# Kernel tuning notes

Measured on AMD Instinct MI355X. Metric: run time of the kernel, lower is better.

The kernel has to match this reference:

```python
import jax, jax.numpy as jnp
import numpy as np

LEAKY_SLOPE = 0.01  # torch nn.LeakyReLU default


def leaky_relu(x):
    return jnp.where(x >= 0, x, LEAKY_SLOPE * x)


def rgcn_conv(x, edge_index, edge_type, w_rel, w_root, b_conv):
    # PyG RGCNConv: out = x @ W_root + b + sum_r mean_{edges of rel r into i}(x_src @ W_r)
    n = x.shape[0]
    src, dst = edge_index[0], edge_index[1]
    out = x @ w_root + b_conv
    num_rel = w_rel.shape[0]
    for r in range(num_rel):  # small fixed relation count
        mask = (edge_type == r)
        msg = x[src] @ w_rel[r]                      # [E, H]
        msg = jnp.where(mask[:, None], msg, 0.0)
        agg = jax.ops.segment_sum(msg, dst, num_segments=n)          # [N, H]
        cnt = jax.ops.segment_sum(mask.astype(x.dtype), dst, num_segments=n)
        out = out + agg / jnp.maximum(cnt, 1.0)[:, None]             # mean aggr
    return out


def setup_inputs() -> dict:
    key = jax.random.key(0)
    ks = jax.random.split(key, 10)
    N, E, D_IN, H, OUT, R = 50000, 600000, 768, 128, 3, 2
    s_in = 1.0 / np.sqrt(D_IN)
    s_h = 1.0 / np.sqrt(H)
    return {
        "feature": jax.random.normal(ks[0], (N, D_IN), dtype=jnp.float32),
        "edge_index": jax.random.randint(ks[1], (2, E), 0, N, dtype=jnp.int64),
        "edge_type": jax.random.randint(ks[2], (E,), 0, R, dtype=jnp.int64),
        "w_in": jax.random.uniform(ks[3], (D_IN, H), jnp.float32, -s_in, s_in),
        "b_in": jax.random.uniform(ks[4], (H,), jnp.float32, -s_in, s_in),
        "w_rel": jax.random.uniform(ks[5], (R, H, H), jnp.float32, -s_h, s_h),
        "w_root": jax.random.uniform(ks[6], (H, H), jnp.float32, -s_h, s_h),
        "b_conv": jnp.zeros((H,), jnp.float32),
        "w_out": jax.random.uniform(ks[7], (H, OUT), jnp.float32, -s_h, s_h),
        "b_out": jax.random.uniform(ks[8], (OUT,), jnp.float32, -s_h, s_h),
    }


def reference(feature, edge_index, edge_type, w_in, b_in, w_rel, w_root, b_conv, w_out, b_out):
    x = leaky_relu(feature @ w_in + b_in)
    # NOTE: original forward applies rgcn1 twice (shared weights); dropout is
    # identity at inference; rgcn2/linear_relu_output1 are unused.
    x = rgcn_conv(x, edge_index, edge_type, w_rel, w_root, b_conv)
    x = rgcn_conv(x, edge_index, edge_type, w_rel, w_root, b_conv)
    return x @ w_out + b_out
```

## Files before the change

### kernel.cpp

```cpp
#include <hip/hip_runtime.h>

#define H 128
#define CAP 64

typedef _Float16 f16x8 __attribute__((ext_vector_type(8)));
typedef float    f32x4 __attribute__((ext_vector_type(4)));

__global__ __launch_bounds__(256) void hist_fill(const int* __restrict__ src,
    const int* __restrict__ dst, const int* __restrict__ et,
    int* __restrict__ cnt, int* __restrict__ elist, int E, int N)
{
    int e = blockIdx.x * 256 + threadIdx.x;
    if (e >= E) return;
    int s = src[e], d = dst[e], t = et[e];
    int b = t * N + d;
    int pos = atomicAdd(&cnt[b], 1);
    if (pos < CAP) elist[(size_t)b * CAP + pos] = s;
}

__global__ __launch_bounds__(256) void prep_w(const float* __restrict__ w_in,
    const float* __restrict__ w_root, const float* __restrict__ w_rel,
    _Float16* __restrict__ wInT, _Float16* __restrict__ w3T, int K)
{
    int idx = blockIdx.x * 256 + threadIdx.x;
    int tot1 = K * H;
    if (idx < tot1) {
        int c = idx / K, k = idx - c * K;
        wInT[idx] = (_Float16)w_in[(size_t)k * H + c];
    } else {
        int i2 = idx - tot1;
        if (i2 < 3 * H * H) {
            int m = i2 / (H * H), r2 = i2 - m * (H * H);
            int c = r2 >> 7, k = r2 & 127;
            const float* s = (m == 0) ? w_root : (w_rel + (size_t)(m - 1) * H * H);
            w3T[i2] = (_Float16)s[(size_t)k * H + c];
        }
    }
}

__device__ __forceinline__ f16x8 cvt8(float4 v0, float4 v1) {
    f16x8 t;
    t[0] = (_Float16)v0.x; t[1] = (_Float16)v0.y; t[2] = (_Float16)v0.z; t[3] = (_Float16)v0.w;
    t[4] = (_Float16)v1.x; t[5] = (_Float16)v1.y; t[6] = (_Float16)v1.z; t[7] = (_Float16)v1.w;
    return t;
}

__global__ __launch_bounds__(256, 4) void gemm_big(const float* __restrict__ A,
    const _Float16* __restrict__ WT, const float* __restrict__ bias,
    _Float16* __restrict__ C16, int M, int K)
{
    __shared__ _Float16 As[2][64][40];
    __shared__ _Float16 Bs[2][128][40];

    const int tid = threadIdx.x;
    const int bm  = blockIdx.x * 64;
    const int w   = tid >> 6;
    const int l   = tid & 63;
    const int l15 = l & 15;
    const int q   = l >> 4;
    const int wr  = (w & 1) * 32;
    const int wc  = (w >> 1) * 64;

    const int sar = tid >> 2;
    const int sak = (tid & 3) * 8;
    int sarow = bm + sar; if (sarow >= M) sarow = M - 1;
    const float* ap = A + (size_t)sarow * K + sak;
    const int sbc = tid >> 1;
    const int sbk = (tid & 1) * 16;
    const _Float16* wp = WT + (size_t)sbc * K + sbk;

    f32x4 acc[2][4];
    const f32x4 z4 = {0.f, 0.f, 0.f, 0.f};
#pragma unroll
    for (int i = 0; i < 2; i++)
#pragma unroll
        for (int j = 0; j < 4; j++) acc[i][j] = z4;

    {
        float4 a0 = *(const float4*)(ap);
        float4 a1 = *(const float4*)(ap + 4);
        f16x8 b0  = *(const f16x8*)(wp);
        f16x8 b1  = *(const f16x8*)(wp + 8);
        *(f16x8*)&As[0][sar][sak]     = cvt8(a0, a1);
        *(f16x8*)&Bs[0][sbc][sbk]     = b0;
        *(f16x8*)&Bs[0][sbc][sbk + 8] = b1;
    }
    __syncthreads();

    const int steps = K / 32;
#pragma unroll 2
    for (int s = 0; s < steps; s++) {
        const int cur = s & 1;
        const bool more = (s + 1) < steps;
        float4 na0, na1; f16x8 nb0, nb1;
        if (more) {
            const int k0 = (s + 1) * 32;
            na0 = *(const float4*)(ap + k0);
            na1 = *(const float4*)(ap + k0 + 4);
            nb0 = *(const f16x8*)(wp + k0);
            nb1 = *(const f16x8*)(wp + k0 + 8);
        }
        f16x8 af[2], bf[4];
#pragma unroll
        for (int i = 0; i < 2; i++) af[i] = *(const f16x8*)&As[cur][wr + i * 16 + l15][q * 8];
#pragma unroll
        for (int j = 0; j < 4; j++) bf[j] = *(const f16x8*)&Bs[cur][wc + j * 16 + l15][q * 8];
#pragma unroll
        for (int i = 0; i < 2; i++)
#pragma unroll
            for (int j = 0; j < 4; j++)
                acc[i][j] = __builtin_amdgcn_mfma_f32_16x16x32_f16(af[i], bf[j], acc[i][j], 0, 0, 0);
        if (more) {
            *(f16x8*)&As[cur ^ 1][sar][sak]     = cvt8(na0, na1);
            *(f16x8*)&Bs[cur ^ 1][sbc][sbk]     = nb0;
            *(f16x8*)&Bs[cur ^ 1][sbc][sbk + 8] = nb1;
        }
        __syncthreads();
    }

#pragma unroll
    for (int j = 0; j < 4; j++) {
        int col = wc + j * 16 + l15;
        float bj = bias[col];
#pragma unroll
        for (int i = 0; i < 2; i++)
#pragma unroll
            for (int rg = 0; rg < 4; rg++) {
                int row = bm + wr + i * 16 + q * 4 + rg;
                if (row < M) {
                    float v = acc[i][j][rg] + bj;
                    v = (v >= 0.f) ? v : 0.01f * v;
                    C16[(size_t)row * H + col] = (_Float16)v;
                }
            }
    }
}

__global__ __launch_bounds__(512) void gemm3(const _Float16* __restrict__ X16,
    const _Float16* __restrict__ W3, const float* __restrict__ bias,
    float* __restrict__ Y, _Float16* __restrict__ Hh, int M, int mtiles,
    size_t NH)
{
    const int w   = threadIdx.x >> 6;
    const int l   = threadIdx.x & 63;
    const int l15 = l & 15;
    const int q   = l >> 4;
    const int col = w * 16 + l15;

    f16x8 bf[3][4];
#pragma unroll
    for (int m = 0; m < 3; m++) {
        const _Float16* wpp = W3 + (size_t)m * H * H + (size_t)col * H + q * 8;
#pragma unroll
        for (int c = 0; c < 4; c++) bf[m][c] = *(const f16x8*)(wpp + c * 32);
    }
    const float bj = bias[col];

    int t = blockIdx.x;
    if (t >= mtiles) return;
    f16x8 xf[4];
    {
        const _Float16* xp = X16 + ((size_t)t * 16 + l15) * H + q * 8;
#pragma unroll
        for (int c = 0; c < 4; c++) xf[c] = *(const f16x8*)(xp + c * 32);
    }

    const f32x4 z4 = {0.f, 0.f, 0.f, 0.f};
    while (true) {
        int tn = t + gridDim.x;
        bool more = tn < mtiles;
        f16x8 xnf[4];
        if (more) {
            const _Float16* xp = X16 + ((size_t)tn * 16 + l15) * H + q * 8;
#pragma unroll
            for (int c = 0; c < 4; c++) xnf[c] = *(const f16x8*)(xp + c * 32);
        }

        f32x4 a0 = z4, a1 = z4, a2 = z4;
#pragma unroll
        for (int c = 0; c < 4; c++) {
            a0 = __builtin_amdgcn_mfma_f32_16x16x32_f16(xf[c], bf[0][c], a0, 0, 0, 0);
            a1 = __builtin_amdgcn_mfma_f32_16x16x32_f16(xf[c], bf[1][c], a1, 0, 0, 0);
            a2 = __builtin_amdgcn_mfma_f32_16x16x32_f16(xf[c], bf[2][c], a2, 0, 0, 0);
        }

#pragma unroll
        for (int rg = 0; rg < 4; rg++) {
            int row = t * 16 + q * 4 + rg;
            if (row < M) {
                Y [(size_t)row * H + col]      = a0[rg] + bj;
                Hh[(size_t)row * H + col]      = (_Float16)a1[rg];
                Hh[NH + (size_t)row * H + col] = (_Float16)a2[rg];
            }
        }
        if (!more) break;
        t = tn;
#pragma unroll
        for (int c = 0; c < 4; c++) xf[c] = xnf[c];
    }
}

__global__ __launch_bounds__(256) void gather_mean(const float* __restrict__ Y,
    const _Float16* __restrict__ h, const int* __restrict__ elist,
    const int* __restrict__ cnt, _Float16* __restrict__ xn, int N, size_t NH)
{
    int wv = blockIdx.x * 4 + (threadIdx.x >> 6);
    int l  = threadIdx.x & 63;
    if (wv >= N) return;

    int d0r = cnt[wv], d1r = cnt[N + wv];
    int d0 = d0r < CAP ? d0r : CAP;
    int d1 = d1r < CAP ? d1r : CAP;
    float inv0 = d0r > 0 ? 1.f / (float)d0r : 0.f;
    float inv1 = d1r > 0 ? 1.f / (float)d1r : 0.f;
    const int* l0 = elist + (size_t)wv * CAP;
    const int* l1 = elist + ((size_t)N + wv) * CAP;
    const int tot = d0 + d1;

    const int eo = l >> 4;
    const int c8 = (l & 15) * 8;

    float acc[8];
#pragma unroll
    for (int j = 0; j < 8; j++) acc[j] = 0.f;

    for (int p = eo; p < tot; p += 8) {
        int pb = p + 4;
        bool fA = p < d0;
        int   sA  = fA ? l0[p] : l1[p - d0];
        float scA = fA ? inv0 : inv1;
        size_t hA = fA ? (size_t)0 : NH;
        f16x8 vA  = *(const f16x8*)&h[hA + (size_t)sA * H + c8];
        if (pb < tot) {
            bool fB = pb < d0;
            int   sB  = fB ? l0[pb] : l1[pb - d0];
            float scB = fB ? inv0 : inv1;
            size_t hB = fB ? (size_t)0 : NH;
            f16x8 vB  = *(const f16x8*)&h[hB + (size_t)sB * H + c8];
#pragma unroll
            for (int j = 0; j < 8; j++) acc[j] += scA * (float)vA[j] + scB * (float)vB[j];
        } else {
#pragma unroll
            for (int j = 0; j < 8; j++) acc[j] += scA * (float)vA[j];
        }
    }

#pragma unroll
    for (int j = 0; j < 8; j++) {
        acc[j] += __shfl_xor(acc[j], 16);
        acc[j] += __shfl_xor(acc[j], 32);
    }

    if (eo == 0) {
        float4 y0 = *(const float4*)&Y[(size_t)wv * H + c8];
        float4 y1 = *(const float4*)&Y[(size_t)wv * H + c8 + 4];
        f16x8 o;
        o[0] = (_Float16)(acc[0] + y0.x); o[1] = (_Float16)(acc[1] + y0.y);
        o[2] = (_Float16)(acc[2] + y0.z); o[3] = (_Float16)(acc[3] + y0.w);
        o[4] = (_Float16)(acc[4] + y1.x); o[5] = (_Float16)(acc[5] + y1.y);
        o[6] = (_Float16)(acc[6] + y1.z); o[7] = (_Float16)(acc[7] + y1.w);
        *(f16x8*)&xn[(size_t)wv * H + c8] = o;
    }
}

__global__ __launch_bounds__(256) void out_gemm(const _Float16* __restrict__ X16,
    const float* __restrict__ Wo, const float* __restrict__ bo,
    float* __restrict__ out, int N, int OUT)
{
    int row = blockIdx.x * 4 + (threadIdx.x >> 6);
    int lane = threadIdx.x & 63;
    if (row >= N) return;
    float a0 = (float)X16[(size_t)row * H + lane];
    float a1 = (float)X16[(size_t)row * H + 64 + lane];
    for (int c = 0; c < OUT; c++) {
        float p = a0 * Wo[lane * OUT + c] + a1 * Wo[(64 + lane) * OUT + c];
        for (int off = 32; off > 0; off >>= 1) p += __shfl_down(p, off);
        if (lane == 0) out[(size_t)row * OUT + c] = p + bo[c];
    }
}

extern "C" void kernel_launch(void* const* d_in, const int* in_sizes, int n_in,
                              void* d_out, int out_size, void* d_ws, size_t ws_size,
                              hipStream_t stream) {
    const float* feature = (const float*)d_in[0];
    const int*   ei      = (const int*)d_in[1];
    const int*   et      = (const int*)d_in[2];
    const float* w_in    = (const float*)d_in[3];
    const float* b_in    = (const float*)d_in[4];
    const float* w_rel   = (const float*)d_in[5];
    const float* w_root  = (const float*)d_in[6];
    const float* b_conv  = (const float*)d_in[7];
    const float* w_out   = (const float*)d_in[8];
    const float* b_out   = (const float*)d_in[9];

    const int HH   = in_sizes[4];
    const int D_IN = in_sizes[3] / HH;
    const int N    = in_sizes[0] / D_IN;
    const int E    = in_sizes[1] / 2;
    const int R    = in_sizes[5] / (HH * HH);
    const int OUT  = in_sizes[9];

    const size_t NH = (size_t)N * H;

    char* base = (char*)d_ws;
    _Float16* wInT = (_Float16*)base;
    _Float16* w3T  = wInT + (size_t)D_IN * HH;
    _Float16* x0   = w3T + (size_t)3 * HH * HH;
    _Float16* x1   = x0 + NH;
    _Float16* h    = x1 + NH;
    float* y       = (float*)(h + (size_t)R * NH);
    int* cnt       = (int*)(y + NH);
    int* elist     = cnt + (size_t)R * N;

    hipMemsetAsync(cnt, 0, sizeof(int) * (size_t)R * N, stream);
    prep_w<<<(D_IN * HH + 3 * HH * HH + 255) / 256, 256, 0, stream>>>(
        w_in, w_root, w_rel, wInT, w3T, D_IN);
    hist_fill<<<(E + 255) / 256, 256, 0, stream>>>(ei, ei + E, et, cnt, elist, E, N);

    gemm_big<<<(N + 63) / 64, 256, 0, stream>>>(feature, wInT, b_in, x0, N, D_IN);

    const int mtiles = (N + 15) / 16;
    _Float16* xc = x0;
    _Float16* xo = x1;
    for (int layer = 0; layer < 2; layer++) {
        gemm3<<<1024, 512, 0, stream>>>(xc, w3T, b_conv, y, h, N, mtiles, NH);
        gather_mean<<<(N + 3) / 4, 256, 0, stream>>>(y, h, elist, cnt, xo, N, NH);
        _Float16* t = xc; xc = xo; xo = t;
    }

    out_gemm<<<(N + 3) / 4, 256, 0, stream>>>(xc, w_out, b_out, (float*)d_out, N, OUT);
}
```

Before: 464.8 us.

## Split-K input GEMM with LDS-resident weight half and separate reduce kernel

Reworks the first dense GEMM so each 1024-thread block holds one K-half of the transposed weight in shared memory. Each wave streams its A rows straight from global memory into registers, so the A tile is no longer staged through LDS and no per-step barriers are needed. Each block writes fp32 partial sums for its K-half, and a new reduce kernel adds the two halves, applies bias and LeakyReLU, and converts to fp16. This removes the LDS double-buffer for A and the repeated weight reloads, at the cost of writing and reading two fp32 N×H partial buffers plus one extra launch.

```diff
diff --git a/kernel.cpp b/kernel.cpp
--- a/kernel.cpp
+++ b/kernel.cpp
@@ -2,6 +2,7 @@
 
 #define H 128
 #define CAP 64
+#define BSTRIDE 392
 
 typedef _Float16 f16x8 __attribute__((ext_vector_type(8)));
 typedef float    f32x4 __attribute__((ext_vector_type(4)));
@@ -45,95 +46,98 @@
     return t;
 }
 
-__global__ __launch_bounds__(256, 4) void gemm_big(const float* __restrict__ A,
-    const _Float16* __restrict__ WT, const float* __restrict__ bias,
-    _Float16* __restrict__ C16, int M, int K)
-{
-    __shared__ _Float16 As[2][64][40];
-    __shared__ _Float16 Bs[2][128][40];
-
-    const int tid = threadIdx.x;
-    const int bm  = blockIdx.x * 64;
+__global__ __launch_bounds__(1024, 4) void gemm_big(const float* __restrict__ A,
+    const _Float16* __restrict__ WT, float* __restrict__ P,
+    int M, int K, size_t NH)
+{
+    __shared__ _Float16 Bsh[128 * BSTRIDE];
+
+    const int khalf = blockIdx.x & 1;
+    const int rt    = blockIdx.x >> 1;
+    const int KH    = K >> 1;
+    const int tid   = threadIdx.x;
+
+    {
+        const int col = tid >> 3;
+        const int seg = tid & 7;
+        const _Float16* srcp = WT + (size_t)col * K + khalf * KH + seg * 8;
+        _Float16* dstp = &Bsh[col * BSTRIDE + seg * 8];
+        for (int k = 0; k < KH; k += 64)
+            *(f16x8*)(dstp + k) = *(const f16x8*)(srcp + k);
+    }
+    __syncthreads();
+
     const int w   = tid >> 6;
     const int l   = tid & 63;
     const int l15 = l & 15;
     const int q   = l >> 4;
-    const int wr  = (w & 1) * 32;
-    const int wc  = (w >> 1) * 64;
-
-    const int sar = tid >> 2;
-    const int sak = (tid & 3) * 8;
-    int sarow = bm + sar; if (sarow >= M) sarow = M - 1;
-    const float* ap = A + (size_t)sarow * K + sak;
-    const int sbc = tid >> 1;
-    const int sbk = (tid & 1) * 16;
-    const _Float16* wp = WT + (size_t)sbc * K + sbk;
-
-    f32x4 acc[2][4];
+
+    int arow = rt * 256 + w * 16 + l15;
+    if (arow >= M) arow = M - 1;
+    const float* ap = A + (size_t)arow * K + khalf * KH + q * 8;
+
+    f32x4 acc[8];
     const f32x4 z4 = {0.f, 0.f, 0.f, 0.f};
 #pragma unroll
-    for (int i = 0; i < 2; i++)
-#pragma unroll
-        for (int j = 0; j < 4; j++) acc[i][j] = z4;
-
-    {
-        float4 a0 = *(const float4*)(ap);
-        float4 a1 = *(const float4*)(ap + 4);
-        f16x8 b0  = *(const f16x8*)(wp);
-        f16x8 b1  = *(const f16x8*)(wp + 8);
-        *(f16x8*)&As[0][sar][sak]     = cvt8(a0, a1);
-        *(f16x8*)&Bs[0][sbc][sbk]     = b0;
-        *(f16x8*)&Bs[0][sbc][sbk + 8] = b1;
-    }
-    __syncthreads();
-
-    const int steps = K / 32;
+    for (int j = 0; j < 8; j++) acc[j] = z4;
+
+    const int chunks = KH >> 5;
+    float4 a0 = *(const float4*)(ap);
+    float4 a1 = *(const float4*)(ap + 4);
 #pragma unroll 2
-    for (int s = 0; s < steps; s++) {
-        const int cur = s & 1;
-        const bool more = (s + 1) < steps;
-        float4 na0, na1; f16x8 nb0, nb1;
-        if (more) {
-            const int k0 = (s + 1) * 32;
-            na0 = *(const float4*)(ap + k0);
-            na1 = *(const float4*)(ap + k0 + 4);
-            nb0 = *(const f16x8*)(wp + k0);
-            nb1 = *(const f16x8*)(wp + k0 + 8);
-        }
-        f16x8 af[2], bf[4];
-#pragma unroll
-        for (int i = 0; i < 2; i++) af[i] = *(const f16x8*)&As[cur][wr + i * 16 + l15][q * 8];
-#pragma unroll
-        for (int j = 0; j < 4; j++) bf[j] = *(const f16x8*)&Bs[cur][wc + j * 16 + l15][q * 8];
-#pragma unroll
-        for (int i = 0; i < 2; i++)
-#pragma unroll
-            for (int j = 0; j < 4; j++)
-                acc[i][j] = __builtin_amdgcn_mfma_f32_16x16x32_f16(af[i], bf[j], acc[i][j], 0, 0, 0);
-        if (more) {
-            *(f16x8*)&As[cur ^ 1][sar][sak]     = cvt8(na0, na1);
-            *(f16x8*)&Bs[cur ^ 1][sbc][sbk]     = nb0;
-            *(f16x8*)&Bs[cur ^ 1][sbc][sbk + 8] = nb1;
-        }
-        __syncthreads();
-    }
-
-#pragma unroll
-    for (int j = 0; j < 4; j++) {
-        int col = wc + j * 16 + l15;
-        float bj = bias[col];
-#pragma unroll
-        for (int i = 0; i < 2; i++)
-#pragma unroll
-            for (int rg = 0; rg < 4; rg++) {
-                int row = bm + wr + i * 16 + q * 4 + rg;
-                if (row < M) {
-                    float v = acc[i][j][rg] + bj;
-                    v = (v >= 0.f) ? v : 0.01f * v;
-                    C16[(size_t)row * H + col] = (_Float16)v;
-                }
-            }
-    }
+    for (int c = 0; c < chunks; c++) {
+        float4 n0, n1;
+        if (c + 1 < chunks) {
+            n0 = *(const float4*)(ap + (c + 1) * 32);
+            n1 = *(const float4*)(ap + (c + 1) * 32 + 4);
+        }
+        f16x8 af = cvt8(a0, a1);
+        const _Float16* bbase = &Bsh[l15 * BSTRIDE + c * 32 + q * 8];
+#pragma unroll
+        for (int j = 0; j < 8; j++) {
+            f16x8 bf = *(const f16x8*)(bbase + j * 16 * BSTRIDE);
+            acc[j] = __builtin_amdgcn_mfma_f32_16x16x32_f16(af, bf, acc[j], 0, 0, 0);
+        }
+        a0 = n0; a1 = n1;
+    }
+
+    float* Pb = P + (size_t)khalf * NH;
+#pragma unroll
+    for (int j = 0; j < 8; j++) {
+        int col = j * 16 + l15;
+#pragma unroll
+        for (int rg = 0; rg < 4; rg++) {
+            int row = rt * 256 + w * 16 + q * 4 + rg;
+            if (row < M) Pb[(size_t)row * H + col] = acc[j][rg];
+        }
+    }
+}
+
+__global__ __launch_bounds__(256) void reduce_x(const float* __restrict__ P,
+    const float* __restrict__ b, _Float16* __restrict__ x0, int total8, size_t NH)
+{
+    int i = blockIdx.x * 256 + threadIdx.x;
+    if (i >= total8) return;
+    size_t off = (size_t)i * 8;
+    float4 p00 = *(const float4*)(P + off);
+    float4 p01 = *(const float4*)(P + off + 4);
+    float4 p10 = *(const float4*)(P + NH + off);
+    float4 p11 = *(const float4*)(P + NH + off + 4);
+    int colb = (int)(off & (H - 1));
+    float4 b0 = *(const float4*)(b + colb);
+    float4 b1 = *(const float4*)(b + colb + 4);
+    float v[8] = {p00.x + p10.x + b0.x, p00.y + p10.y + b0.y,
+                  p00.z + p10.z + b0.z, p00.w + p10.w + b0.w,
+                  p01.x + p11.x + b1.x, p01.y + p11.y + b1.y,
+                  p01.z + p11.z + b1.z, p01.w + p11.w + b1.w};
+    f16x8 o;
+#pragma unroll
+    for (int k = 0; k < 8; k++) {
+        float t = v[k];
+        t = (t >= 0.f) ? t : 0.01f * t;
+        o[k] = (_Float16)t;
+    }
+    *(f16x8*)&x0[off] = o;
 }
 
 __global__ __launch_bounds__(512) void gemm3(const _Float16* __restrict__ X16,
@@ -309,7 +313,8 @@
     _Float16* x1   = x0 + NH;
     _Float16* h    = x1 + NH;
     float* y       = (float*)(h + (size_t)R * NH);
-    int* cnt       = (int*)(y + NH);
+    float* P       = y + NH;
+    int* cnt       = (int*)(P + 2 * NH);
     int* elist     = cnt + (size_t)R * N;
 
     hipMemsetAsync(cnt, 0, sizeof(int) * (size_t)R * N, stream);
@@ -317,7 +322,9 @@
         w_in, w_root, w_rel, wInT, w3T, D_IN);
     hist_fill<<<(E + 255) / 256, 256, 0, stream>>>(ei, ei + E, et, cnt, elist, E, N);
 
-    gemm_big<<<(N + 63) / 64, 256, 0, stream>>>(feature, wInT, b_in, x0, N, D_IN);
+    const int rgroups = (N + 255) / 256;
+    gemm_big<<<2 * rgroups, 1024, 0, stream>>>(feature, wInT, P, N, D_IN, NH);
+    reduce_x<<<(N * (H / 8) + 255) / 256, 256, 0, stream>>>(P, b_in, x0, N * (H / 8), NH);
 
     const int mtiles = (N + 15) / 16;
     _Float16* xc = x0;
```

After: 466.6 us. About the same (+0.4%).
